# Kernel tuning notes

Hardware: AMD Instinct MI355X
Metric: run time of the kernel (lower is better)

The kernel has to match this reference:

```python
import jax, jax.numpy as jnp
import numpy as np

H = 512  # hidden_size

def _gru_layer(x_tbf, Wih, Whh, bih, bhh):
    # x_tbf: (T, B, F). PyTorch GRU cell:
    # r = sig(Wir x + bir + Whr h + bhr); z = sig(Wiz x + biz + Whz h + bhz)
    B = x_tbf.shape[1]
    gx = jnp.einsum('tbf,gf->tbg', x_tbf, Wih) + bih  # (T, B, 3H), precomputed input gates
    def step(h, gx_t):
        gh = h @ Whh.T + bhh  # (B, 3H)
        r = jax.nn.sigmoid(gx_t[:, :H] + gh[:, :H])
        z = jax.nn.sigmoid(gx_t[:, H:2*H] + gh[:, H:2*H])
        n = jnp.tanh(gx_t[:, 2*H:] + r * gh[:, 2*H:])
        h_new = (1.0 - z) * n + z * h
        return h_new, h_new
    h0 = jnp.zeros((B, H), dtype=x_tbf.dtype)
    hT, ys = jax.lax.scan(step, h0, gx)
    return ys, hT  # (T, B, H), (B, H)


def setup_inputs() -> dict:
    key = jax.random.key(0)
    ks = jax.random.split(key, 12)
    B, T, I, O = 32, 1024, 128, 128
    k = 1.0 / np.sqrt(H)
    u = lambda kk, shape: jax.random.uniform(kk, shape, jnp.float32, -k, k)
    return {
        'x': jax.random.normal(ks[0], (B, T, I), jnp.float32),
        'Wih0': u(ks[1], (3 * H, I)),
        'Whh0': u(ks[2], (3 * H, H)),
        'bih0': u(ks[3], (3 * H,)),
        'bhh0': u(ks[4], (3 * H,)),
        'Wih1': u(ks[5], (3 * H, H)),
        'Whh1': u(ks[6], (3 * H, H)),
        'bih1': u(ks[7], (3 * H,)),
        'bhh1': u(ks[8], (3 * H,)),
        'Wout': u(ks[9], (O, H)),
        'bout': u(ks[10], (O,)),
    }


def reference(x, Wih0, Whh0, bih0, bhh0, Wih1, Whh1, bih1, bhh1, Wout, bout):
    x_tbf = jnp.transpose(x, (1, 0, 2))  # (T, B, I)
    y0, h0T = _gru_layer(x_tbf, Wih0, Whh0, bih0, bhh0)
    y1, h1T = _gru_layer(y0, Wih1, Whh1, bih1, bhh1)
    # Linear output applied at every timestep
    out = jnp.einsum('tbh,oh->bto', y1, Wout) + bout  # (B, T, O)
    hidden = jnp.stack([h0T, h1T], axis=0)  # (n_layers, B, H)
    return out, hidden
```

## Files before the change

### kernel.cpp

```cpp
#include <hip/hip_runtime.h>


typedef __attribute__((ext_vector_type(8))) short short8;
typedef __attribute__((ext_vector_type(4))) float floatx4;

#define MFMA_BF16(a, b, c) __builtin_amdgcn_mfma_f32_16x16x32_bf16(a, b, c, 0, 0, 0)

#define NWG 130
#define EX_REC 132096
#define EX_OUT 66560
#define HBUF_REC (EX_REC + 24576)
#define LDS_BYTES 157696
#define HID_OFF 4194304
#define SLOT 32768

__device__ __align__(16) unsigned g_flags[256];
__device__ __align__(16) unsigned short g_y0[33587200];
__device__ __align__(16) unsigned short g_y1[33587200];
__device__ __align__(16) unsigned short g_xf[8388608];

static __device__ __forceinline__ float bf2f(unsigned short u) {
  unsigned v = ((unsigned)u) << 16;
  return __builtin_bit_cast(float, v);
}
static __device__ __forceinline__ unsigned short f2bf(float f) {
  unsigned u = __builtin_bit_cast(unsigned, f);
  u = (u + 0x7fffu + ((u >> 16) & 1u)) >> 16;
  return (unsigned short)u;
}
static __device__ __forceinline__ float sigf(float x) {
  return 1.f / (1.f + __expf(-x));
}
static __device__ __forceinline__ void st8(unsigned short* p, unsigned long long v) {
  __hip_atomic_store((unsigned long long*)p, v, __ATOMIC_RELAXED,
                     __HIP_MEMORY_SCOPE_AGENT);
}
static __device__ __forceinline__ unsigned long long pack4(const unsigned short* u) {
  return (unsigned long long)u[0] | ((unsigned long long)u[1] << 16) |
         ((unsigned long long)u[2] << 32) | ((unsigned long long)u[3] << 48);
}
static __device__ __forceinline__ void ldfrag(const unsigned short* slot, int kb,
                                              int t, int lane, short8& hi,
                                              short8& lo) {
  const unsigned short* base = slot + (kb * 2 + t) * 1024 + lane * 8;
  hi = *(const short8*)base;
  lo = *(const short8*)(base + 512);
}

extern "C" __global__ void gru_init() {
  int i = blockIdx.x * blockDim.x + threadIdx.x;
  if (i < 256) {
    g_flags[i] = 0u;
  } else if (i < 16640) {
    ((unsigned*)g_y0)[i - 256] = 0u;
  } else if (i < 33024) {
    ((unsigned*)g_y1)[i - 16640] = 0u;
  }
}

extern "C" __global__ void x_arrange(const float* __restrict__ x) {
  int gid = blockIdx.x * 256 + threadIdx.x;
  int t = gid >> 9;
  int rem = gid & 511;
  int kb = rem >> 7;
  int tile = (rem >> 6) & 1;
  int lane = rem & 63;
  int b = tile * 16 + (lane & 15);
  int k = kb * 32 + (lane >> 4) * 8;
  const float* src = x + b * 131072 + t * 128 + k;
  short8 hi, lo;
#pragma unroll
  for (int e = 0; e < 8; ++e) {
    float v = src[e];
    unsigned short h = f2bf(v);
    hi[e] = (short)h;
    lo[e] = (short)f2bf(v - bf2f(h));
  }
  unsigned short* dst = g_xf + ((t * 4 + kb) * 2 + tile) * 1024;
  *(short8*)(dst + lane * 8) = hi;
  *(short8*)(dst + 512 + lane * 8) = lo;
}

template <int LAYER>
__device__ __forceinline__ void layer_step(
    int i, int tid, int q, int lane, int jb,
    const unsigned short* whi, const unsigned short* wlo, float* ex, float* hbuf,
    float* __restrict__ dout,
    float bsr, float bsz, float bin, float bhn, float& hp) {
  constexpr int IHK = LAYER ? 512 : 128;
  constexpr int IHS = IHK / 32;
  constexpr int KSW = LAYER ? 8 : 5;
  constexpr int WSTR = IHK + 512 + 8;
  const int lm = lane & 15, lq = lane >> 4;

  const unsigned short* ihs = LAYER ? (g_y0 + (size_t)i * SLOT) : nullptr;
  const unsigned short* hhs =
      LAYER ? (g_y1 + (size_t)(i - 1) * SLOT) : (g_y0 + (size_t)i * SLOT);

  const floatx4 z4 = {0.f, 0.f, 0.f, 0.f};
  floatx4 t0h[2] = {z4, z4}, t0l[2] = {z4, z4};
  floatx4 tih_h[2] = {z4, z4}, tih_l[2] = {z4, z4};
  floatx4 thh_h[2] = {z4, z4}, thh_l[2] = {z4, z4};

#pragma unroll
  for (int s = 0; s < KSW; ++s) {
    int ks = q * KSW + s;
    int colk = ks * 32 + lq * 8;
    short8 ah[2], al[2];
    if (ks < IHS) {
      if (LAYER == 0) {
        const unsigned short* xb = g_xf + (i * 4 + ks) * 2048;
        ah[0] = *(const short8*)(xb + lane * 8);
        al[0] = *(const short8*)(xb + 512 + lane * 8);
        ah[1] = *(const short8*)(xb + 1024 + lane * 8);
        al[1] = *(const short8*)(xb + 1536 + lane * 8);
      } else {
        ldfrag(ihs, ks, 0, lane, ah[0], al[0]);
        ldfrag(ihs, ks, 1, lane, ah[1], al[1]);
      }
    } else {
      ldfrag(hhs, ks - IHS, 0, lane, ah[0], al[0]);
      ldfrag(hhs, ks - IHS, 1, lane, ah[1], al[1]);
    }
    short8 b0h = *(const short8*)(whi + lm * WSTR + colk);
    short8 b0l = *(const short8*)(wlo + lm * WSTR + colk);
    short8 b1h = *(const short8*)(whi + (16 + lm) * WSTR + colk);
    short8 b1l = *(const short8*)(wlo + (16 + lm) * WSTR + colk);
#pragma unroll
    for (int t = 0; t < 2; ++t) {
      t0h[t] = MFMA_BF16(ah[t], b0h, t0h[t]);
      t0l[t] = MFMA_BF16(ah[t], b0l, t0l[t]);
      t0l[t] = MFMA_BF16(al[t], b0h, t0l[t]);
      if (ks < IHS) {
        tih_h[t] = MFMA_BF16(ah[t], b1h, tih_h[t]);
        tih_l[t] = MFMA_BF16(ah[t], b1l, tih_l[t]);
        tih_l[t] = MFMA_BF16(al[t], b1h, tih_l[t]);
      } else {
        thh_h[t] = MFMA_BF16(ah[t], b1h, thh_h[t]);
        thh_l[t] = MFMA_BF16(ah[t], b1l, thh_l[t]);
        thh_l[t] = MFMA_BF16(al[t], b1h, thh_l[t]);
      }
    }
  }
#pragma unroll
  for (int t = 0; t < 2; ++t) {
    *(floatx4*)(ex + ((0 * 4 + q) * 2 + t) * 256 + lane * 4) = t0h[t] + t0l[t];
    *(floatx4*)(ex + ((1 * 4 + q) * 2 + t) * 256 + lane * 4) = tih_h[t] + tih_l[t];
    *(floatx4*)(ex + ((2 * 4 + q) * 2 + t) * 256 + lane * 4) = thh_h[t] + thh_l[t];
  }
  __syncthreads();

  int m = tid >> 3, j = tid & 7;
  int quad = (m >> 2) & 3, reg = m & 3, mh = m >> 4;
  int offr = (quad * 16 + j) * 4 + reg;
  int offz = (quad * 16 + 8 + j) * 4 + reg;
  float sr = 0, sz = 0, sih = 0, shh = 0;
#pragma unroll
  for (int qq = 0; qq < 4; ++qq) {
    const float* s0 = ex + ((0 * 4 + qq) * 2 + mh) * 256;
    const float* s1 = ex + ((1 * 4 + qq) * 2 + mh) * 256;
    const float* s2 = ex + ((2 * 4 + qq) * 2 + mh) * 256;
    sr += s0[offr];
    sz += s0[offz];
    sih += s1[offr];
    shh += s2[offr];
  }
  float r = sigf(sr + bsr);
  float z = sigf(sz + bsz);
  float n = tanhf(sih + bin + r * (shh + bhn));
  float h = (1.f - z) * n + z * hp;
  hp = h;
  hbuf[m * 8 + j] = h;
  if (i == (LAYER ? 1024 : 1023))
    dout[HID_OFF + LAYER * 16384 + m * 512 + jb + j] = h;
  __syncthreads();

  if (tid < 32) {
    int mm = tid;
    int t = mm >> 4;
    int lanep = (mm & 15) + 16 * ((jb >> 3) & 3);
    int kb = jb >> 5;
    unsigned short h4[8], l4[8];
#pragma unroll
    for (int e = 0; e < 8; ++e) {
      float v = hbuf[mm * 8 + e];
      unsigned short hh = f2bf(v);
      h4[e] = hh;
      l4[e] = f2bf(v - bf2f(hh));
    }
    unsigned short* slot =
        LAYER ? (g_y1 + (size_t)i * SLOT) : (g_y0 + (size_t)(i + 1) * SLOT);
    unsigned short* p = slot + (kb * 2 + t) * 1024 + lanep * 8;
    st8(p, pack4(h4));
    st8(p + 4, pack4(h4 + 4));
    st8(p + 512, pack4(l4));
    st8(p + 516, pack4(l4 + 4));
  }
}

__device__ __forceinline__ void out_step(
    int i, int tid, int lane, int q, int ob,
    const unsigned short* wl, float* ex,
    float* __restrict__ dout, const float* bo) {
  const int lm = lane & 15, lq = lane >> 4;
  const unsigned short* slot = g_y1 + (size_t)(i - 1) * SLOT;
  const floatx4 z4 = {0.f, 0.f, 0.f, 0.f};
  floatx4 acc[4][2];
#pragma unroll
  for (int nt = 0; nt < 4; ++nt) { acc[nt][0] = z4; acc[nt][1] = z4; }
#pragma unroll
  for (int s = 0; s < 4; ++s) {
    int ks = q * 4 + s;
    int colk = ks * 32 + lq * 8;
    short8 a0 = *(const short8*)(slot + (ks * 2 + 0) * 1024 + lane * 8);
    short8 a1 = *(const short8*)(slot + (ks * 2 + 1) * 1024 + lane * 8);
#pragma unroll
    for (int nt = 0; nt < 4; ++nt) {
      short8 b = *(const short8*)(wl + (nt * 16 + lm) * 520 + colk);
      acc[nt][0] = MFMA_BF16(a0, b, acc[nt][0]);
      acc[nt][1] = MFMA_BF16(a1, b, acc[nt][1]);
    }
  }
#pragma unroll
  for (int nt = 0; nt < 4; ++nt) {
    *(floatx4*)(ex + ((q * 4 + nt) * 2 + 0) * 256 + lane * 4) = acc[nt][0];
    *(floatx4*)(ex + ((q * 4 + nt) * 2 + 1) * 256 + lane * 4) = acc[nt][1];
  }
  __syncthreads();
  int m = tid >> 3, oc = (tid & 7) * 8;
  int t_out = i - 2;
  float sv[8];
#pragma unroll
  for (int k = 0; k < 8; ++k) {
    int o = oc + k;
    int nt = o >> 4, jj = o & 15;
    int off = (((m >> 2) & 3) * 16 + jj) * 4 + (m & 3);
    int mh = m >> 4;
    float s = bo[k];
#pragma unroll
    for (int qq = 0; qq < 4; ++qq) s += ex[((qq * 4 + nt) * 2 + mh) * 256 + off];
    sv[k] = s;
  }
  float* dst = dout + m * 131072 + t_out * 128 + ob + oc;
  *(floatx4*)dst = floatx4{sv[0], sv[1], sv[2], sv[3]};
  *(floatx4*)(dst + 4) = floatx4{sv[4], sv[5], sv[6], sv[7]};
}

extern "C" __global__ void __launch_bounds__(256, 1) gru_main(
    const float* __restrict__ Wih0, const float* __restrict__ Whh0,
    const float* __restrict__ bih0, const float* __restrict__ bhh0,
    const float* __restrict__ Wih1, const float* __restrict__ Whh1,
    const float* __restrict__ bih1, const float* __restrict__ bhh1,
    const float* __restrict__ Wout, const float* __restrict__ boutp,
    float* __restrict__ dout) {
  extern __shared__ char smem[];
  __shared__ int sbail;

  int* flags = (int*)g_flags;

  const int w = blockIdx.x;
  const int tid = threadIdx.x;
  const int lane = tid & 63;
  const int q = tid >> 6;
  const int role = (w < 128) ? ((w < 64) ? 0 : 1) : 2;

  if (tid == 0) sbail = 0;

  unsigned short* whi = (unsigned short*)smem;
  float* ex = (float*)(smem + (role == 2 ? EX_OUT : EX_REC));
  float* hbuf = (float*)(smem + HBUF_REC);
  {
    int exn = (role == 2) ? 8192 : 6144;
    for (int idx = tid; idx < exn; idx += 256) ex[idx] = 0.f;
  }

  float bsr = 0, bsz = 0, bin = 0, bhn = 0;
  float bo[8] = {0, 0, 0, 0, 0, 0, 0, 0};
  int jb = 0, ob = 0;
  const unsigned short* wlo = nullptr;

  if (role < 2) {
    jb = (role == 0 ? w : w - 64) * 8;
    const int IHK = role ? 512 : 128;
    const int KTOT = IHK + 512;
    const int WSTR = KTOT + 8;
    unsigned short* wlo_w = whi + 32 * WSTR;
    wlo = wlo_w;
    const float* Wih = role ? Wih1 : Wih0;
    const float* Whh = role ? Whh1 : Whh0;
    const float* bih = role ? bih1 : bih0;
    const float* bhh = role ? bhh1 : bhh0;
    int cpr = KTOT / 8;
    for (int idx = tid; idx < 32 * cpr; idx += 256) {
      int r = idx / cpr, c = idx - r * cpr;
      int k0 = c * 8;
      short8 hi8 = {0, 0, 0, 0, 0, 0, 0, 0}, lo8 = {0, 0, 0, 0, 0, 0, 0, 0};
      if (r < 24) {
        int gate = r >> 3, jl = r & 7;
        int grow = gate * 512 + jb + jl;
        const float* src = (k0 < IHK) ? (Wih + grow * IHK + k0)
                                      : (Whh + grow * 512 + (k0 - IHK));
#pragma unroll
        for (int e = 0; e < 8; ++e) {
          float v = src[e];
          unsigned short h16 = f2bf(v);
          hi8[e] = (short)h16;
          lo8[e] = (short)f2bf(v - bf2f(h16));
        }
      }
      *(short8*)(whi + r * WSTR + k0) = hi8;
      *(short8*)(wlo_w + r * WSTR + k0) = lo8;
    }
    for (int idx = tid; idx < 32 * 8; idx += 256) {
      int r = idx >> 3, kk = KTOT + (idx & 7);
      whi[r * WSTR + kk] = 0;
      wlo_w[r * WSTR + kk] = 0;
    }
    int g0 = jb + (tid & 7);
    bsr = bih[g0] + bhh[g0];
    bsz = bih[512 + g0] + bhh[512 + g0];
    bin = bih[1024 + g0];
    bhn = bhh[1024 + g0];
  } else {
    ob = (w - 128) * 64;
    for (int idx = tid; idx < 64 * 64; idx += 256) {
      int r = idx >> 6, c = idx & 63;
      const float* src = Wout + (ob + r) * 512 + c * 8;
      short8 hi8;
#pragma unroll
      for (int e = 0; e < 8; ++e) hi8[e] = (short)f2bf(src[e]);
      *(short8*)(whi + r * 520 + c * 8) = hi8;
    }
    for (int idx = tid; idx < 64 * 8; idx += 256)
      whi[(idx >> 3) * 520 + 512 + (idx & 7)] = 0;
#pragma unroll
    for (int k = 0; k < 8; ++k) bo[k] = boutp[ob + (tid & 7) * 8 + k];
  }
  __builtin_amdgcn_fence(__ATOMIC_ACQUIRE, "agent");
  __syncthreads();

  float hp = 0.f;

  for (int i = 0; i < 1026; ++i) {
    if (i > 0 && tid < 64) {
      int guard = 0;
      for (;;) {
        bool ok;
        if (role == 0) {
          ok = __hip_atomic_load(flags + tid, __ATOMIC_RELAXED,
                                 __HIP_MEMORY_SCOPE_AGENT) >= i;
        } else if (role == 1) {
          ok = (__hip_atomic_load(flags + tid, __ATOMIC_RELAXED,
                                  __HIP_MEMORY_SCOPE_AGENT) >= i) &&
               (__hip_atomic_load(flags + 64 + tid, __ATOMIC_RELAXED,
                                  __HIP_MEMORY_SCOPE_AGENT) >= i);
        } else {
          ok = __hip_atomic_load(flags + 64 + tid, __ATOMIC_RELAXED,
                                 __HIP_MEMORY_SCOPE_AGENT) >= i;
        }
        if (__ballot(ok) == ~0ull) break;
        __builtin_amdgcn_s_sleep(1);
        if (++guard > (1 << 17)) { sbail = 1; break; }
      }
    }
    __syncthreads();
    if (sbail) break;

    bool active = (role == 0) ? (i < 1024)
                : (role == 1) ? (i >= 1 && i < 1025)
                              : (i >= 2);
    if (active) {
      if (role == 0) {
        layer_step<0>(i, tid, q, lane, jb, whi, wlo, ex, hbuf, dout,
                      bsr, bsz, bin, bhn, hp);
      } else if (role == 1) {
        layer_step<1>(i, tid, q, lane, jb, whi, wlo, ex, hbuf, dout,
                      bsr, bsz, bin, bhn, hp);
      } else {
        out_step(i, tid, lane, q, ob, whi, ex, dout, bo);
      }
    }
    __syncthreads();
    if (tid == 0)
      __hip_atomic_store(&flags[w], i + 1, __ATOMIC_RELAXED,
                         __HIP_MEMORY_SCOPE_AGENT);
  }
}

extern "C" void kernel_launch(void* const* d_in, const int* in_sizes, int n_in,
                              void* d_out, int out_size, void* d_ws, size_t ws_size,
                              hipStream_t stream) {
  const float* x = (const float*)d_in[0];
  const float* Wih0 = (const float*)d_in[1];
  const float* Whh0 = (const float*)d_in[2];
  const float* bih0 = (const float*)d_in[3];
  const float* bhh0 = (const float*)d_in[4];
  const float* Wih1 = (const float*)d_in[5];
  const float* Whh1 = (const float*)d_in[6];
  const float* bih1 = (const float*)d_in[7];
  const float* bhh1 = (const float*)d_in[8];
  const float* Wout = (const float*)d_in[9];
  const float* bout = (const float*)d_in[10];

  hipLaunchKernelGGL(gru_init, dim3(129), dim3(256), 0, stream);
  hipLaunchKernelGGL(x_arrange, dim3(524288 / 256), dim3(256), 0, stream, x);

  hipFuncSetAttribute((const void*)gru_main,
                      hipFuncAttributeMaxDynamicSharedMemorySize, LDS_BYTES);
  hipLaunchKernelGGL(gru_main, dim3(NWG), dim3(256), LDS_BYTES, stream,
                     Wih0, Whh0, bih0, bhh0, Wih1, Whh1, bih1, bhh1, Wout,
                     bout, (float*)d_out);
}
```

Baseline: 7.207 ms.

## Replace per-step flag barriers with sentinel-valued data polling

Removes the global flag array and the per-step spin-wait on producer flags. Consumers now load their hidden-state fragments with atomic 8-byte loads and re-poll any word still holding a 0xFFFF sentinel, so data arrival itself acts as the synchronization. The init kernel now has to fill both full ring buffers (about 134 MB) with sentinels, which adds a large memset-like cost. It also relies on 8-byte atomic store granularity and on a real bf16 value never equalling the sentinel pattern.

```diff
diff --git a/kernel.cpp b/kernel.cpp
--- a/kernel.cpp
+++ b/kernel.cpp
@@ -13,8 +13,8 @@
 #define LDS_BYTES 157696
 #define HID_OFF 4194304
 #define SLOT 32768
-
-__device__ __align__(16) unsigned g_flags[256];
+#define SENT16 0xFFFFull
+
 __device__ __align__(16) unsigned short g_y0[33587200];
 __device__ __align__(16) unsigned short g_y1[33587200];
 __device__ __align__(16) unsigned short g_xf[8388608];
@@ -35,26 +35,25 @@
   __hip_atomic_store((unsigned long long*)p, v, __ATOMIC_RELAXED,
                      __HIP_MEMORY_SCOPE_AGENT);
 }
+static __device__ __forceinline__ unsigned long long lda8(const unsigned short* p) {
+  return __hip_atomic_load((const unsigned long long*)p, __ATOMIC_RELAXED,
+                           __HIP_MEMORY_SCOPE_AGENT);
+}
 static __device__ __forceinline__ unsigned long long pack4(const unsigned short* u) {
   return (unsigned long long)u[0] | ((unsigned long long)u[1] << 16) |
          ((unsigned long long)u[2] << 32) | ((unsigned long long)u[3] << 48);
 }
-static __device__ __forceinline__ void ldfrag(const unsigned short* slot, int kb,
-                                              int t, int lane, short8& hi,
-                                              short8& lo) {
-  const unsigned short* base = slot + (kb * 2 + t) * 1024 + lane * 8;
-  hi = *(const short8*)base;
-  lo = *(const short8*)(base + 512);
-}
 
 extern "C" __global__ void gru_init() {
-  int i = blockIdx.x * blockDim.x + threadIdx.x;
-  if (i < 256) {
-    g_flags[i] = 0u;
-  } else if (i < 16640) {
-    ((unsigned*)g_y0)[i - 256] = 0u;
-  } else if (i < 33024) {
-    ((unsigned*)g_y1)[i - 16640] = 0u;
+  const int N4 = 4198400;
+  uint4 sent; sent.x = sent.y = sent.z = sent.w = 0xFFFFFFFFu;
+  uint4 zero; zero.x = zero.y = zero.z = zero.w = 0u;
+  for (int idx = blockIdx.x * 256 + threadIdx.x; idx < 2 * N4;
+       idx += gridDim.x * 256) {
+    int ring = idx >= N4;
+    int k = ring ? idx - N4 : idx;
+    uint4* base = (uint4*)(ring ? g_y1 : g_y0);
+    base[k] = (k < 4096) ? zero : sent;
   }
 }
 
@@ -97,6 +96,68 @@
   const unsigned short* hhs =
       LAYER ? (g_y1 + (size_t)(i - 1) * SLOT) : (g_y0 + (size_t)i * SLOT);
 
+  unsigned long long vw[KSW][2][4];
+  const unsigned short* bp[KSW][2];
+  bool need[KSW];
+#pragma unroll
+  for (int s = 0; s < KSW; ++s) {
+    int ks = q * KSW + s;
+    if (LAYER == 0 && ks < IHS) {
+      const unsigned short* xb = g_xf + (i * 4 + ks) * 2048;
+      union { short8 s8; unsigned long long u[2]; } a0, b0, a1, b1;
+      a0.s8 = *(const short8*)(xb + lane * 8);
+      b0.s8 = *(const short8*)(xb + 512 + lane * 8);
+      a1.s8 = *(const short8*)(xb + 1024 + lane * 8);
+      b1.s8 = *(const short8*)(xb + 1536 + lane * 8);
+      vw[s][0][0] = a0.u[0]; vw[s][0][1] = a0.u[1];
+      vw[s][0][2] = b0.u[0]; vw[s][0][3] = b0.u[1];
+      vw[s][1][0] = a1.u[0]; vw[s][1][1] = a1.u[1];
+      vw[s][1][2] = b1.u[0]; vw[s][1][3] = b1.u[1];
+      need[s] = false;
+      bp[s][0] = nullptr; bp[s][1] = nullptr;
+    } else {
+      const unsigned short* sl;
+      int kbb;
+      if (ks < IHS) { sl = ihs; kbb = ks; } else { sl = hhs; kbb = ks - IHS; }
+#pragma unroll
+      for (int t = 0; t < 2; ++t) {
+        const unsigned short* b = sl + (kbb * 2 + t) * 1024 + lane * 8;
+        bp[s][t] = b;
+        vw[s][t][0] = lda8(b);
+        vw[s][t][1] = lda8(b + 4);
+        vw[s][t][2] = lda8(b + 512);
+        vw[s][t][3] = lda8(b + 516);
+      }
+      need[s] = true;
+    }
+  }
+  {
+    int guard = 0;
+    for (;;) {
+      bool bad = false;
+#pragma unroll
+      for (int s = 0; s < KSW; ++s) {
+        if (!need[s]) continue;
+#pragma unroll
+        for (int t = 0; t < 2; ++t) {
+#pragma unroll
+          for (int wd = 0; wd < 4; ++wd) {
+            if ((vw[s][t][wd] & 0xFFFFull) == SENT16) {
+              const unsigned short* b =
+                  bp[s][t] + (wd == 1 ? 4 : wd == 2 ? 512 : wd == 3 ? 516 : 0);
+              vw[s][t][wd] = lda8(b);
+              bad = true;
+            }
+          }
+        }
+      }
+      if (!bad) break;
+      __builtin_amdgcn_s_sleep(1);
+      if (++guard > (1 << 17)) break;
+    }
+    asm volatile("" ::: "memory");
+  }
+
   const floatx4 z4 = {0.f, 0.f, 0.f, 0.f};
   floatx4 t0h[2] = {z4, z4}, t0l[2] = {z4, z4};
   floatx4 tih_h[2] = {z4, z4}, tih_l[2] = {z4, z4};
@@ -107,20 +168,13 @@
     int ks = q * KSW + s;
     int colk = ks * 32 + lq * 8;
     short8 ah[2], al[2];
-    if (ks < IHS) {
-      if (LAYER == 0) {
-        const unsigned short* xb = g_xf + (i * 4 + ks) * 2048;
-        ah[0] = *(const short8*)(xb + lane * 8);
-        al[0] = *(const short8*)(xb + 512 + lane * 8);
-        ah[1] = *(const short8*)(xb + 1024 + lane * 8);
-        al[1] = *(const short8*)(xb + 1536 + lane * 8);
-      } else {
-        ldfrag(ihs, ks, 0, lane, ah[0], al[0]);
-        ldfrag(ihs, ks, 1, lane, ah[1], al[1]);
-      }
-    } else {
-      ldfrag(hhs, ks - IHS, 0, lane, ah[0], al[0]);
-      ldfrag(hhs, ks - IHS, 1, lane, ah[1], al[1]);
+#pragma unroll
+    for (int t = 0; t < 2; ++t) {
+      union { unsigned long long u[2]; short8 s8; } ua, ub;
+      ua.u[0] = vw[s][t][0]; ua.u[1] = vw[s][t][1];
+      ub.u[0] = vw[s][t][2]; ub.u[1] = vw[s][t][3];
+      ah[t] = ua.s8;
+      al[t] = ub.s8;
     }
     short8 b0h = *(const short8*)(whi + lm * WSTR + colk);
     short8 b0l = *(const short8*)(wlo + lm * WSTR + colk);
@@ -201,9 +255,44 @@
 __device__ __forceinline__ void out_step(
     int i, int tid, int lane, int q, int ob,
     const unsigned short* wl, float* ex,
-    float* __restrict__ dout, const float* bo) {
+    float* __restrict__ dout, const float* bov) {
   const int lm = lane & 15, lq = lane >> 4;
   const unsigned short* slot = g_y1 + (size_t)(i - 1) * SLOT;
+
+  unsigned long long vo[4][2][2];
+  const unsigned short* bp[4][2];
+#pragma unroll
+  for (int s = 0; s < 4; ++s) {
+    int ks = q * 4 + s;
+#pragma unroll
+    for (int t = 0; t < 2; ++t) {
+      const unsigned short* b = slot + (ks * 2 + t) * 1024 + lane * 8;
+      bp[s][t] = b;
+      vo[s][t][0] = lda8(b);
+      vo[s][t][1] = lda8(b + 4);
+    }
+  }
+  {
+    int guard = 0;
+    for (;;) {
+      bool bad = false;
+#pragma unroll
+      for (int s = 0; s < 4; ++s)
+#pragma unroll
+        for (int t = 0; t < 2; ++t)
+#pragma unroll
+          for (int wd = 0; wd < 2; ++wd)
+            if ((vo[s][t][wd] & 0xFFFFull) == SENT16) {
+              vo[s][t][wd] = lda8(bp[s][t] + (wd ? 4 : 0));
+              bad = true;
+            }
+      if (!bad) break;
+      __builtin_amdgcn_s_sleep(1);
+      if (++guard > (1 << 17)) break;
+    }
+    asm volatile("" ::: "memory");
+  }
+
   const floatx4 z4 = {0.f, 0.f, 0.f, 0.f};
   floatx4 acc[4][2];
 #pragma unroll
@@ -212,8 +301,10 @@
   for (int s = 0; s < 4; ++s) {
     int ks = q * 4 + s;
     int colk = ks * 32 + lq * 8;
-    short8 a0 = *(const short8*)(slot + (ks * 2 + 0) * 1024 + lane * 8);
-    short8 a1 = *(const short8*)(slot + (ks * 2 + 1) * 1024 + lane * 8);
+    union { unsigned long long u[2]; short8 s8; } u0, u1;
+    u0.u[0] = vo[s][0][0]; u0.u[1] = vo[s][0][1];
+    u1.u[0] = vo[s][1][0]; u1.u[1] = vo[s][1][1];
+    short8 a0 = u0.s8, a1 = u1.s8;
 #pragma unroll
     for (int nt = 0; nt < 4; ++nt) {
       short8 b = *(const short8*)(wl + (nt * 16 + lm) * 520 + colk);
@@ -236,7 +327,7 @@
     int nt = o >> 4, jj = o & 15;
     int off = (((m >> 2) & 3) * 16 + jj) * 4 + (m & 3);
     int mh = m >> 4;
-    float s = bo[k];
+    float s = bov[k];
 #pragma unroll
     for (int qq = 0; qq < 4; ++qq) s += ex[((qq * 4 + nt) * 2 + mh) * 256 + off];
     sv[k] = s;
@@ -254,17 +345,12 @@
     const float* __restrict__ Wout, const float* __restrict__ boutp,
     float* __restrict__ dout) {
   extern __shared__ char smem[];
-  __shared__ int sbail;
-
-  int* flags = (int*)g_flags;
 
   const int w = blockIdx.x;
   const int tid = threadIdx.x;
   const int lane = tid & 63;
   const int q = tid >> 6;
   const int role = (w < 128) ? ((w < 64) ? 0 : 1) : 2;
-
-  if (tid == 0) sbail = 0;
 
   unsigned short* whi = (unsigned short*)smem;
   float* ex = (float*)(smem + (role == 2 ? EX_OUT : EX_REC));
@@ -342,30 +428,6 @@
   float hp = 0.f;
 
   for (int i = 0; i < 1026; ++i) {
-    if (i > 0 && tid < 64) {
-      int guard = 0;
-      for (;;) {
-        bool ok;
-        if (role == 0) {
-          ok = __hip_atomic_load(flags + tid, __ATOMIC_RELAXED,
-                                 __HIP_MEMORY_SCOPE_AGENT) >= i;
-        } else if (role == 1) {
-          ok = (__hip_atomic_load(flags + tid, __ATOMIC_RELAXED,
-                                  __HIP_MEMORY_SCOPE_AGENT) >= i) &&
-               (__hip_atomic_load(flags + 64 + tid, __ATOMIC_RELAXED,
-                                  __HIP_MEMORY_SCOPE_AGENT) >= i);
-        } else {
-          ok = __hip_atomic_load(flags + 64 + tid, __ATOMIC_RELAXED,
-                                 __HIP_MEMORY_SCOPE_AGENT) >= i;
-        }
-        if (__ballot(ok) == ~0ull) break;
-        __builtin_amdgcn_s_sleep(1);
-        if (++guard > (1 << 17)) { sbail = 1; break; }
-      }
-    }
-    __syncthreads();
-    if (sbail) break;
-
     bool active = (role == 0) ? (i < 1024)
                 : (role == 1) ? (i >= 1 && i < 1025)
                               : (i >= 2);
@@ -381,9 +443,6 @@
       }
     }
     __syncthreads();
-    if (tid == 0)
-      __hip_atomic_store(&flags[w], i + 1, __ATOMIC_RELAXED,
-                         __HIP_MEMORY_SCOPE_AGENT);
   }
 }
 
@@ -402,7 +461,7 @@
   const float* Wout = (const float*)d_in[9];
   const float* bout = (const float*)d_in[10];
 
-  hipLaunchKernelGGL(gru_init, dim3(129), dim3(256), 0, stream);
+  hipLaunchKernelGGL(gru_init, dim3(4096), dim3(256), 0, stream);
   hipLaunchKernelGGL(x_arrange, dim3(524288 / 256), dim3(256), 0, stream, x);
 
   hipFuncSetAttribute((const void*)gru_main,
```

Result: slower. 7.816 ms (+8.4%).
